# Optimization experiments

Hardware: AMD Instinct MI355X
Metric: run time of the kernel (lower is better)

Reference implementation:

```python
import jax, jax.numpy as jnp
import numpy as np

NUM_SAMPLED = 8192
NUM_CLASSES = 50000
DIM = 512
BATCH = 8192


def _log_uniform_expected(ids, num_sampled, num_classes):
    # log-uniform sampler probability: P(c) = (log(c+2) - log(c+1)) / log(V+1)
    c = ids.astype(jnp.float32)
    p = (jnp.log(c + 2.0) - jnp.log(c + 1.0)) / jnp.log(float(num_classes + 1))
    # expected count under unique sampling of num_sampled candidates (as in TF)
    return -jnp.expm1(float(num_sampled) * jnp.log1p(-p))


def setup_inputs() -> dict:
    key = jax.random.key(0)
    k1, k2, k3, k4, k5 = jax.random.split(key, 5)
    inputs = jax.random.normal(k1, (BATCH, DIM), jnp.float32)
    labels = jax.random.randint(k2, (BATCH, 1), 0, NUM_CLASSES)
    kernel = jax.random.uniform(k3, (NUM_CLASSES, DIM), jnp.float32, -0.05, 0.05)
    bias = jax.random.uniform(k4, (NUM_CLASSES,), jnp.float32, -0.05, 0.05)
    sampled = jax.random.randint(k5, (NUM_SAMPLED,), 0, NUM_CLASSES)
    return {"inputs": inputs, "labels": labels, "kernel": kernel,
            "bias": bias, "sampled": sampled}


def reference(inputs, labels, kernel, bias, sampled):
    # tf.nn.sampled_softmax_loss (train branch), num_true=1,
    # log-uniform sampler, remove_accidental_hits=True.
    labels_flat = labels[:, 0]

    # true logits: gather one weight row per example, dot with input
    w_true = kernel[labels_flat]                      # [B, D]
    b_true = bias[labels_flat]                        # [B]
    true_logits = jnp.einsum('bd,bd->b', inputs, w_true) + b_true
    true_logits = true_logits - jnp.log(
        _log_uniform_expected(labels_flat, NUM_SAMPLED, NUM_CLASSES))

    # sampled logits: gather S candidate rows, small matmul [B,D]x[D,S]
    w_samp = kernel[sampled]                          # [S, D]
    b_samp = bias[sampled]                            # [S]
    sampled_logits = jnp.einsum('bd,sd->bs', inputs, w_samp) + b_samp[None, :]
    sampled_logits = sampled_logits - jnp.log(
        _log_uniform_expected(sampled, NUM_SAMPLED, NUM_CLASSES))

    # remove accidental hits: mask sampled candidates that equal the true label
    hits = labels_flat[:, None] == sampled[None, :]   # [B, S]
    sampled_logits = jnp.where(hits, -1e9, sampled_logits)

    # softmax CE with the true class at column 0
    logits = jnp.concatenate([true_logits[:, None], sampled_logits], axis=1)
    loss = jax.nn.logsumexp(logits, axis=1) - logits[:, 0]  # [B]
    return loss
```

## Files before the change

kernel.cpp:

```cpp
#include <hip/hip_runtime.h>
#include <hip/hip_bf16.h>
#include <cstdint>
#include <cstddef>

#define BATCH   8192
#define NSAMP   8192
#define DIM     512
#define NCLASS  50000

typedef __attribute__((ext_vector_type(8))) short bf16x8;
typedef __attribute__((ext_vector_type(4))) float f32x4;

__device__ __forceinline__ float neg_log_expected(int c) {
    double p = log1p(1.0 / (double)(c + 1)) / log((double)(NCLASS + 1));
    double e = -expm1((double)NSAMP * log1p(-p));
    return (float)(-log(e));
}

__device__ __forceinline__ unsigned short f2bf(float f) {
    __hip_bfloat16 h = __float2bfloat16(f);
    return *reinterpret_cast<unsigned short*>(&h);
}

__device__ __forceinline__ void gload_lds16(const void* g, void* l) {
    __builtin_amdgcn_global_load_lds(
        (const __attribute__((address_space(1))) void*)g,
        (__attribute__((address_space(3))) void*)l, 16, 0, 0);
}

__global__ void k_fused(const float* __restrict__ inputs, const int* __restrict__ labels,
                        const float* __restrict__ W, const float* __restrict__ bias,
                        __hip_bfloat16* __restrict__ Abf,
                        float* __restrict__ true_logit, float* __restrict__ row_sum) {
    int row = blockIdx.x;
    int t   = threadIdx.x;
    float4 v = reinterpret_cast<const float4*>(inputs + (size_t)row * DIM)[t];
    ushort4 u;
    u.x = f2bf(v.x); u.y = f2bf(v.y); u.z = f2bf(v.z); u.w = f2bf(v.w);
    reinterpret_cast<ushort4*>(Abf + (size_t)row * DIM)[t] = u;

    int lbl = labels[row];
    float4 w = reinterpret_cast<const float4*>(W + (size_t)lbl * DIM)[t];
    float dot = v.x * w.x + v.y * w.y + v.z * w.z + v.w * w.w;
    #pragma unroll
    for (int off = 32; off; off >>= 1) dot += __shfl_down(dot, off, 64);
    __shared__ float red[2];
    if ((t & 63) == 0) red[t >> 6] = dot;
    __syncthreads();
    if (t == 0) {
        float tl = red[0] + red[1] + bias[lbl] + neg_log_expected(lbl);
        true_logit[row] = tl;
        row_sum[row]    = __expf(tl);
    }
}

__global__ void k_gather(const float* __restrict__ W, const float* __restrict__ bias,
                         const int* __restrict__ sampled,
                         __hip_bfloat16* __restrict__ Bbf, float* __restrict__ adj) {
    int s   = blockIdx.x;
    int idx = sampled[s];
    float4 v = reinterpret_cast<const float4*>(W + (size_t)idx * DIM)[threadIdx.x];
    ushort4 u;
    u.x = f2bf(v.x); u.y = f2bf(v.y); u.z = f2bf(v.z); u.w = f2bf(v.w);
    reinterpret_cast<ushort4*>(Bbf + (size_t)s * DIM)[threadIdx.x] = u;
    if (threadIdx.x == 0) adj[s] = bias[idx] + neg_log_expected(idx);
}


#define BARRIER() asm volatile("s_barrier" ::: "memory")
#define VMCNT(n)  asm volatile("s_waitcnt vmcnt(" #n ")" ::: "memory")

#define READ_A(BUF, MH)                                                        \
    _Pragma("unroll")                                                          \
    for (int mi = 0; mi < 4; ++mi)                                             \
      _Pragma("unroll")                                                        \
      for (int ks = 0; ks < 2; ++ks)                                           \
        af[mi][ks] = *reinterpret_cast<const bf16x8*>(                         \
          &Asm[BUF][abase + ((MH)*4 + mi)*2048 + (((ks*4) + gg) ^ axg)*8]);

#define READ_B(BUF, NH)                                                        \
    _Pragma("unroll")                                                          \
    for (int ni = 0; ni < 2; ++ni)                                             \
      _Pragma("unroll")                                                        \
      for (int ks = 0; ks < 2; ++ks)                                           \
        bfr[ni][ks] = *reinterpret_cast<const bf16x8*>(                        \
          &Bsm[BUF][bbase + ((NH)*2 + ni)*4096 + (((ks*4) + gg) ^ axg)*8]);

#define MFMA_Q(MH, NH)                                                         \
    __builtin_amdgcn_s_setprio(1);                                             \
    _Pragma("unroll")                                                          \
    for (int mi = 0; mi < 4; ++mi)                                             \
      _Pragma("unroll")                                                        \
      for (int ni = 0; ni < 2; ++ni)                                           \
        _Pragma("unroll")                                                      \
        for (int ks = 0; ks < 2; ++ks)                                         \
          acc[(MH)*4+mi][(NH)*2+ni] = __builtin_amdgcn_mfma_f32_16x16x32_bf16( \
            af[mi][ks], bfr[ni][ks], acc[(MH)*4+mi][(NH)*2+ni], 0, 0, 0);      \
    __builtin_amdgcn_s_setprio(0);

__global__ __launch_bounds__(512, 1) void k_gemm(
    const __hip_bfloat16* __restrict__ A, const __hip_bfloat16* __restrict__ B,
    const float* __restrict__ adj, const int* __restrict__ labels,
    const int* __restrict__ sampled, float* __restrict__ row_sum) {
    __shared__ alignas(16) __hip_bfloat16 Asm[2][256 * 64];
    __shared__ alignas(16) __hip_bfloat16 Bsm[2][256 * 64];
    __shared__ float tsum[4][256];

    const int tid  = threadIdx.x;
    const int wave = tid >> 6;
    const int lane = tid & 63;
    const int wr   = wave >> 2;
    const int wc   = wave & 3;

    int bid = blockIdx.x;
    int wg  = (bid & 7) * 128 + (bid >> 3);
    const int brow = (wg >> 5) * 256;
    const int bcol = (wg & 31) * 256;

    const int sr8 = lane >> 3;
    const int sg8 = (lane & 7) ^ sr8;

    const int rsel  = lane & 15;
    const int gg    = lane >> 4;
    const int axg   = rsel & 7;
    const int abase = (wr * 16 + rsel) * 64;
    const int bbase = (wc * 16 + rsel) * 64;

    f32x4 acc[8][4];
    #pragma unroll
    for (int m = 0; m < 8; ++m)
        #pragma unroll
        for (int n = 0; n < 4; ++n)
            acc[m][n] = (f32x4){0.f, 0.f, 0.f, 0.f};

    auto stageA = [&](int buf, int kt, int half) {
        #pragma unroll
        for (int i = 0; i < 2; ++i) {
            const int lrow = half * 128 + i * 64 + wave * 8;
            const __hip_bfloat16* g =
                A + (size_t)(brow + lrow + sr8) * DIM + kt * 64 + sg8 * 8;
            gload_lds16(g, &Asm[buf][lrow * 64]);
        }
    };
    auto stageB = [&](int buf, int kt, int half) {
        #pragma unroll
        for (int i = 0; i < 2; ++i) {
            const int lrow = half * 128 + i * 64 + wave * 8;
            const __hip_bfloat16* g =
                B + (size_t)(bcol + lrow + sr8) * DIM + kt * 64 + sg8 * 8;
            gload_lds16(g, &Bsm[buf][lrow * 64]);
        }
    };

    stageA(0, 0, 0); stageB(0, 0, 0); stageA(0, 0, 1); stageB(0, 0, 1);

    bf16x8 af[4][2], bfr[2][2];

    #pragma unroll 1
    for (int t = 0; t < 7; ++t) {
        const int buf = t & 1, nb = buf ^ 1, nt = t + 1;
        stageA(nb, nt, 0); VMCNT(6); BARRIER();
        READ_A(buf, 0); READ_B(buf, 0); MFMA_Q(0, 0);
        stageB(nb, nt, 0); VMCNT(6); BARRIER();
        READ_A(buf, 1); MFMA_Q(1, 0);
        stageA(nb, nt, 1); VMCNT(6); BARRIER();
        READ_B(buf, 1); MFMA_Q(1, 1);
        stageB(nb, nt, 1);
        READ_A(buf, 0); MFMA_Q(0, 1);
        BARRIER();
    }
    {
        VMCNT(4); BARRIER();
        READ_A(1, 0); READ_B(1, 0); MFMA_Q(0, 0);
        VMCNT(2); BARRIER();
        READ_A(1, 1); MFMA_Q(1, 0);
        VMCNT(0); BARRIER();
        READ_B(1, 1); MFMA_Q(1, 1);
        READ_A(1, 0); MFMA_Q(0, 1);
    }

    int sv[4]; float aadj[4];
    #pragma unroll
    for (int n = 0; n < 4; ++n) {
        int col = bcol + n * 64 + wc * 16 + rsel;
        aadj[n] = adj[col];
        sv[n]   = sampled[col];
    }
    #pragma unroll
    for (int m = 0; m < 8; ++m) {
        #pragma unroll
        for (int r = 0; r < 4; ++r) {
            int lrow = m * 32 + wr * 16 + gg * 4 + r;
            int lbl  = labels[brow + lrow];
            float part = 0.f;
            #pragma unroll
            for (int n = 0; n < 4; ++n) {
                float logit = acc[m][n][r] + aadj[n];
                part += (sv[n] == lbl) ? 0.f : __expf(logit);
            }
            part += __shfl_xor(part, 1, 16);
            part += __shfl_xor(part, 2, 16);
            part += __shfl_xor(part, 4, 16);
            part += __shfl_xor(part, 8, 16);
            if (rsel == 0) tsum[wc][lrow] = part;
        }
    }
    __syncthreads();
    if (tid < 256)
        atomicAdd(&row_sum[brow + tid],
                  tsum[0][tid] + tsum[1][tid] + tsum[2][tid] + tsum[3][tid]);
}

__global__ void k_final(const float* __restrict__ row_sum,
                        const float* __restrict__ true_logit,
                        float* __restrict__ loss) {
    int i = blockIdx.x * blockDim.x + threadIdx.x;
    loss[i] = logf(row_sum[i]) - true_logit[i];
}

extern "C" void kernel_launch(void* const* d_in, const int* in_sizes, int n_in,
                              void* d_out, int out_size, void* d_ws, size_t ws_size,
                              hipStream_t stream) {
    const float* inputs  = (const float*)d_in[0];
    const int*   labels  = (const int*)d_in[1];
    const float* W       = (const float*)d_in[2];
    const float* bias    = (const float*)d_in[3];
    const int*   sampled = (const int*)d_in[4];
    float*       loss    = (float*)d_out;

    char* ws = (char*)d_ws;
    __hip_bfloat16* Abf = (__hip_bfloat16*)ws;
    __hip_bfloat16* Bbf = (__hip_bfloat16*)(ws + (size_t)BATCH * DIM * 2);
    float* adj        = (float*)(ws + (size_t)(BATCH + NSAMP) * DIM * 2);
    float* true_logit = adj + NSAMP;
    float* row_sum    = true_logit + BATCH;

    hipLaunchKernelGGL(k_fused, dim3(BATCH), dim3(128), 0, stream,
                       inputs, labels, W, bias, Abf, true_logit, row_sum);
    hipLaunchKernelGGL(k_gather, dim3(NSAMP), dim3(128), 0, stream,
                       W, bias, sampled, Bbf, adj);
    hipLaunchKernelGGL(k_gemm, dim3((BATCH / 256) * (NSAMP / 256)), dim3(512), 0, stream,
                       Abf, Bbf, adj, labels, sampled, row_sum);
    hipLaunchKernelGGL(k_final, dim3(BATCH / 256), dim3(256), 0, stream,
                       row_sum, true_logit, loss);
}
```

Measured before the change: 134.3 us.

## Double-buffer B fragments to drop redundant A reload and remap XCD tiles

```diff
diff --git a/kernel.cpp b/kernel.cpp
--- a/kernel.cpp
+++ b/kernel.cpp
@@ -78,15 +78,15 @@
         af[mi][ks] = *reinterpret_cast<const bf16x8*>(                         \
           &Asm[BUF][abase + ((MH)*4 + mi)*2048 + (((ks*4) + gg) ^ axg)*8]);
 
-#define READ_B(BUF, NH)                                                        \
+#define READ_B(BUF, NH, DST)                                                   \
     _Pragma("unroll")                                                          \
     for (int ni = 0; ni < 2; ++ni)                                             \
       _Pragma("unroll")                                                        \
       for (int ks = 0; ks < 2; ++ks)                                           \
-        bfr[ni][ks] = *reinterpret_cast<const bf16x8*>(                        \
+        DST[ni][ks] = *reinterpret_cast<const bf16x8*>(                        \
           &Bsm[BUF][bbase + ((NH)*2 + ni)*4096 + (((ks*4) + gg) ^ axg)*8]);
 
-#define MFMA_Q(MH, NH)                                                         \
+#define MFMA_Q(MH, NH, BSRC)                                                   \
     __builtin_amdgcn_s_setprio(1);                                             \
     _Pragma("unroll")                                                          \
     for (int mi = 0; mi < 4; ++mi)                                             \
@@ -95,7 +95,7 @@
         _Pragma("unroll")                                                      \
         for (int ks = 0; ks < 2; ++ks)                                         \
           acc[(MH)*4+mi][(NH)*2+ni] = __builtin_amdgcn_mfma_f32_16x16x32_bf16( \
-            af[mi][ks], bfr[ni][ks], acc[(MH)*4+mi][(NH)*2+ni], 0, 0, 0);      \
+            af[mi][ks], BSRC[ni][ks], acc[(MH)*4+mi][(NH)*2+ni], 0, 0, 0);     \
     __builtin_amdgcn_s_setprio(0);
 
 __global__ __launch_bounds__(512, 1) void k_gemm(
@@ -112,10 +112,12 @@
     const int wr   = wave >> 2;
     const int wc   = wave & 3;
 
-    int bid = blockIdx.x;
-    int wg  = (bid & 7) * 128 + (bid >> 3);
-    const int brow = (wg >> 5) * 256;
-    const int bcol = (wg & 31) * 256;
+    const int bid   = blockIdx.x;
+    const int xcd   = bid & 7;
+    const int w     = (bid >> 3) & 31;
+    const int rnd   = bid >> 8;
+    const int brow  = ((xcd & 3) * 8 + (w >> 2)) * 256;
+    const int bcol  = (rnd * 8 + (xcd >> 2) * 4 + (w & 3)) * 256;
 
     const int sr8 = lane >> 3;
     const int sg8 = (lane & 7) ^ sr8;
@@ -152,31 +154,31 @@
         }
     };
 
-    stageA(0, 0, 0); stageB(0, 0, 0); stageA(0, 0, 1); stageB(0, 0, 1);
-
-    bf16x8 af[4][2], bfr[2][2];
+    stageA(0, 0, 0); stageB(0, 0, 0); stageB(0, 0, 1); stageA(0, 0, 1);
+
+    bf16x8 af[4][2], bf0[2][2], bf1[2][2];
 
     #pragma unroll 1
     for (int t = 0; t < 7; ++t) {
         const int buf = t & 1, nb = buf ^ 1, nt = t + 1;
         stageA(nb, nt, 0); VMCNT(6); BARRIER();
-        READ_A(buf, 0); READ_B(buf, 0); MFMA_Q(0, 0);
+        READ_A(buf, 0); READ_B(buf, 0, bf0); MFMA_Q(0, 0, bf0);
         stageB(nb, nt, 0); VMCNT(6); BARRIER();
-        READ_A(buf, 1); MFMA_Q(1, 0);
-        stageA(nb, nt, 1); VMCNT(6); BARRIER();
-        READ_B(buf, 1); MFMA_Q(1, 1);
-        stageB(nb, nt, 1);
-        READ_A(buf, 0); MFMA_Q(0, 1);
+        READ_B(buf, 1, bf1); MFMA_Q(0, 1, bf1);
+        stageB(nb, nt, 1); VMCNT(6); BARRIER();
+        READ_A(buf, 1); MFMA_Q(1, 1, bf1);
+        stageA(nb, nt, 1);
+        MFMA_Q(1, 0, bf0);
         BARRIER();
     }
     {
         VMCNT(4); BARRIER();
-        READ_A(1, 0); READ_B(1, 0); MFMA_Q(0, 0);
+        READ_A(1, 0); READ_B(1, 0, bf0); MFMA_Q(0, 0, bf0);
         VMCNT(2); BARRIER();
-        READ_A(1, 1); MFMA_Q(1, 0);
+        READ_B(1, 1, bf1); MFMA_Q(0, 1, bf1);
         VMCNT(0); BARRIER();
-        READ_B(1, 1); MFMA_Q(1, 1);
-        READ_A(1, 0); MFMA_Q(0, 1);
+        READ_A(1, 1); MFMA_Q(1, 1, bf1);
+        MFMA_Q(1, 0, bf0);
     }
 
     int sv[4]; float aadj[4];
```

New measurement: 120.1 us. 1.12x faster.
